# Kernel optimization log

Hardware: AMD Instinct MI355X
Metric: run time of the kernel (lower is better)

The kernel has to match this reference:

```python
import math
import jax, jax.numpy as jnp
import numpy as np

HIDDEN = 768
N_HEADS = 12
HEAD_DIM = HIDDEN // N_HEADS


def _alibi_slopes(num_heads: int) -> np.ndarray:
    def pow2_slopes(n):
        start = 2.0 ** (-2.0 ** (-(math.log2(n) - 3)))
        return start ** np.arange(1, n + 1, dtype=np.float32)
    if math.log2(num_heads).is_integer():
        return pow2_slopes(num_heads).astype(np.float32)
    closest = 2 ** math.floor(math.log2(num_heads))
    base = pow2_slopes(closest)
    extra = pow2_slopes(2 * closest)[0::2][: num_heads - closest]
    return np.concatenate([base, extra], axis=0).astype(np.float32)

ALIBI_SLOPES = jnp.asarray(_alibi_slopes(N_HEADS))


def setup_inputs() -> dict:
    key = jax.random.key(0)
    ks = jax.random.split(key, 7)
    B, S = 4, 2048
    scale = 1.0 / math.sqrt(HIDDEN)
    inp = {
        "hidden_states": jax.random.normal(ks[0], (B, S, HIDDEN), dtype=jnp.float32),
        "Wq": jax.random.normal(ks[1], (HIDDEN, HIDDEN), dtype=jnp.float32) * scale,
        "bq": jnp.zeros((HIDDEN,), dtype=jnp.float32),
        "Wk": jax.random.normal(ks[2], (HIDDEN, HIDDEN), dtype=jnp.float32) * scale,
        "bk": jnp.zeros((HIDDEN,), dtype=jnp.float32),
        "Wv": jax.random.normal(ks[3], (HIDDEN, HIDDEN), dtype=jnp.float32) * scale,
        "bv": jnp.zeros((HIDDEN,), dtype=jnp.float32),
        "attention_mask": jnp.ones((B, S), dtype=jnp.int32),
    }
    return inp


def reference(hidden_states, Wq, bq, Wk, bk, Wv, bv, attention_mask):
    B, S, _ = hidden_states.shape
    H, D = N_HEADS, HEAD_DIM
    scaling = D ** (-0.5)

    # nn.Linear: x @ W.T + b, then split heads -> [B, S, H, D]
    q = (hidden_states @ Wq.T + bq).reshape(B, S, H, D)
    k = (hidden_states @ Wk.T + bk).reshape(B, S, H, D)
    v = (hidden_states @ Vv_fix(Wv, bv, hidden_states)) if False else (hidden_states @ Wv.T + bv).reshape(B, S, H, D)

    # scaled scores [B, H, Sq, Sk]
    scores = jnp.einsum("bqhd,bkhd->bhqk", q, k) * scaling

    # ALiBi bias: -slope[h] * |kv_idx - q_idx|
    pos = jnp.arange(S)
    dist = jnp.abs(pos[None, :] - pos[:, None]).astype(scores.dtype)  # [Sq, Sk]
    alibi = -ALIBI_SLOPES.astype(scores.dtype)[:, None, None] * dist  # [H, Sq, Sk]

    # padding mask over kv positions (additive min like score_mod)
    mask_penalty = jnp.finfo(scores.dtype).min
    mask_bias = jnp.where(attention_mask.astype(bool), 0.0, mask_penalty)  # [B, Sk]

    scores = scores + alibi[None] + mask_bias[:, None, None, :]
    probs = jax.nn.softmax(scores, axis=-1)

    out = jnp.einsum("bhqk,bkhd->bqhd", probs, v)  # [B, Sq, H, D]
    return out.reshape(B, S, H * D)  # dropout is no-op in eval


def Vv_fix(*a):  # unused helper kept trivially (never called)
    raise NotImplementedError
```

## Files before the change

kernel.cpp:

```cpp
#include <hip/hip_runtime.h>
#include <hip/hip_bf16.h>

#define HIDDEN 768
#define NH 12
#define HD 64
#define BB 4
#define SS 2048
#define M_TOT (BB * SS)
#define NQKV (3 * HIDDEN)
#define LOG2E 1.44269504f

typedef __attribute__((ext_vector_type(8))) short bf16x8;
typedef __attribute__((ext_vector_type(4))) float f32x4;
typedef __attribute__((ext_vector_type(4))) unsigned int u32x4;

__device__ inline unsigned short f2bf(float x) {
    __hip_bfloat16 h = __float2bfloat16(x);
    return *reinterpret_cast<unsigned short*>(&h);
}

__device__ inline void gl_lds16(const unsigned short* g, unsigned short* s) {
    __builtin_amdgcn_global_load_lds(
        (const __attribute__((address_space(1))) unsigned int*)g,
        (__attribute__((address_space(3))) unsigned int*)s, 16, 0, 0);
}

__global__ __launch_bounds__(256) void cast_kernel(
    const float* __restrict__ hs, const float* __restrict__ wq,
    const float* __restrict__ wk, const float* __restrict__ wv,
    const int* __restrict__ mask, unsigned short* __restrict__ a_bf,
    unsigned short* __restrict__ w_bf, float* __restrict__ mb,
    int* __restrict__ anym) {
    const int HS_N = M_TOT * HIDDEN / 4;
    const int W_N = HIDDEN * HIDDEN / 4;
    int idx = blockIdx.x * blockDim.x + threadIdx.x;
    if (idx < BB * SS) mb[idx] = mask[idx] ? 0.f : -1e30f;
    if (idx < BB * 32) {
        int b = idx >> 5, t = idx & 31;
        const int* mp = mask + b * SS + t * 64;
        int any = 0;
#pragma unroll 8
        for (int j = 0; j < 64; j++) any |= (mp[j] == 0);
        anym[idx] = any;
    }
    if (idx >= HS_N + 3 * W_N) return;
    if (idx < HS_N) {
        float4 v = ((const float4*)hs)[idx];
        ushort4 o;
        o.x = f2bf(v.x); o.y = f2bf(v.y); o.z = f2bf(v.z); o.w = f2bf(v.w);
        ((ushort4*)a_bf)[idx] = o;
    } else {
        int widx = idx - HS_N;
        const float* src;
        int off;
        if (widx < W_N)        { src = wq; off = widx; }
        else if (widx < 2*W_N) { src = wk; off = widx - W_N; }
        else                   { src = wv; off = widx - 2 * W_N; }
        float4 v = ((const float4*)src)[off];
        ushort4 o;
        o.x = f2bf(v.x); o.y = f2bf(v.y); o.z = f2bf(v.z); o.w = f2bf(v.w);
        ((ushort4*)w_bf)[widx] = o;
    }
}

__global__ __launch_bounds__(256, 3) void qkv_gemm(
    const unsigned short* __restrict__ A, const unsigned short* __restrict__ W,
    const float* __restrict__ bq, const float* __restrict__ bk,
    const float* __restrict__ bv, unsigned short* __restrict__ qbuf,
    unsigned short* __restrict__ kf, unsigned short* __restrict__ vf) {
    __shared__ unsigned short As[2][128][32];
    __shared__ unsigned short Bs[2][128][32];
    const int tid = threadIdx.x;
    const int m0 = blockIdx.y * 128;
    const int n0 = blockIdx.x * 128;
    const int w = tid >> 6, l = tid & 63;
    const int wm = w >> 1, wn = w & 1;
    const int lrow = l & 15;
    const int g4 = l >> 4;
    const int fcol = (g4 ^ (lrow >> 2)) * 8;

    const int srow = l >> 2;
    const int sslot = (l & 3) ^ ((l >> 4) & 3);
    const unsigned short* pA =
        A + (size_t)(m0 + w * 32 + srow) * HIDDEN + sslot * 8;
    const unsigned short* pB =
        W + (size_t)(n0 + w * 32 + srow) * HIDDEN + sslot * 8;

    f32x4 acc[4][4] = {};

#define STAGE(bb)                                          \
    do {                                                   \
        gl_lds16(pA,               &As[bb][w * 32][0]);    \
        gl_lds16(pA + 16 * HIDDEN, &As[bb][w * 32 + 16][0]); \
        gl_lds16(pB,               &Bs[bb][w * 32][0]);    \
        gl_lds16(pB + 16 * HIDDEN, &Bs[bb][w * 32 + 16][0]); \
        pA += 32; pB += 32;                                \
    } while (0)

    STAGE(0);
    __syncthreads();
    int cur = 0;

    for (int kt = 0; kt < HIDDEN / 32; kt++) {
        if (kt < HIDDEN / 32 - 1) STAGE(cur ^ 1);
        bf16x8 af[4], bfr[4];
#pragma unroll
        for (int mi = 0; mi < 4; mi++)
            af[mi] = *(const bf16x8*)&As[cur][wm * 64 + mi * 16 + lrow][fcol];
#pragma unroll
        for (int ni = 0; ni < 4; ni++)
            bfr[ni] = *(const bf16x8*)&Bs[cur][wn * 64 + ni * 16 + lrow][fcol];
        __builtin_amdgcn_s_setprio(1);
#pragma unroll
        for (int mi = 0; mi < 4; mi++)
#pragma unroll
            for (int ni = 0; ni < 4; ni++)
                acc[mi][ni] = __builtin_amdgcn_mfma_f32_16x16x32_bf16(
                    af[mi], bfr[ni], acc[mi][ni], 0, 0, 0);
        __builtin_amdgcn_s_setprio(0);
        __syncthreads();
        cur ^= 1;
    }
#undef STAGE

    if (n0 < 768) {
#pragma unroll
        for (int mi = 0; mi < 4; mi++)
#pragma unroll
            for (int ni = 0; ni < 4; ni++) {
                int col = n0 + wn * 64 + ni * 16 + lrow;
                float bias = bq[col];
#pragma unroll
                for (int i = 0; i < 4; i++) {
                    int row = m0 + wm * 64 + mi * 16 + g4 * 4 + i;
                    qbuf[(size_t)row * 768 + col] =
                        f2bf((acc[mi][ni][i] + bias) * 0.125f);
                }
            }
    } else if (n0 < 1536) {
#pragma unroll
        for (int mi = 0; mi < 4; mi++)
#pragma unroll
            for (int ni = 0; ni < 4; ni++) {
                int dd = n0 - 768 + wn * 64 + ni * 16 + lrow;
                float bias = bk[dd];
                int hh = dd >> 6, d = dd & 63;
                int gk = d >> 3, d8 = d & 7;
#pragma unroll
                for (int i = 0; i < 4; i++) {
                    int row = m0 + wm * 64 + mi * 16 + g4 * 4 + i;
                    int bb2 = row >> 11, s = row & 2047;
                    int kv16 = s >> 4, ls = s & 15;
                    kf[((size_t)(bb2 * NH + hh) * 128 + kv16) * 1024 +
                       (gk * 16 + ls) * 8 + d8] = f2bf(acc[mi][ni][i] + bias);
                }
            }
    } else {
#pragma unroll
        for (int mi = 0; mi < 4; mi++)
#pragma unroll
            for (int ni = 0; ni < 4; ni++) {
                int dd = n0 - 1536 + wn * 64 + ni * 16 + lrow;
                float bias = bv[dd];
                int hh = dd >> 6, d = dd & 63;
                int dm = d >> 4, lr = d & 15;
                int row0 = m0 + wm * 64 + mi * 16 + g4 * 4;
                int bb2 = row0 >> 11, s = row0 & 2047;
                int kv32 = s >> 5, gv = (s >> 3) & 3, s8 = s & 7;
                ushort4 o;
                o.x = f2bf(acc[mi][ni][0] + bias);
                o.y = f2bf(acc[mi][ni][1] + bias);
                o.z = f2bf(acc[mi][ni][2] + bias);
                o.w = f2bf(acc[mi][ni][3] + bias);
                *(ushort4*)(vf + (((size_t)(bb2 * NH + hh) * 4 + dm) * 64 + kv32) * 512 +
                            (gv * 16 + lr) * 8 + s8) = o;
            }
    }
}

__global__ __launch_bounds__(256) void attn_kernel(
    const unsigned short* __restrict__ Qb, const unsigned short* __restrict__ KF,
    const unsigned short* __restrict__ VF, const float* __restrict__ MB,
    const int* __restrict__ ANYM, float* __restrict__ out) {
    __shared__ unsigned short Kl[2][4096];
    __shared__ unsigned short Vl[2][4096];

    const int head_order[12] = {6, 7, 5, 4, 3, 11, 2, 10, 1, 9, 0, 8};
    const int Rtab[12]       = {31, 31, 19, 10, 5, 4, 3, 2, 2, 1, 1, 1};

    const int tid = threadIdx.x;
    const int w = tid >> 6, l = tid & 63;
    const int flat = blockIdx.y * gridDim.x + blockIdx.x;
    const int xcd = flat & 7;
    const int rem = flat >> 3;
    const int slot = rem >> 5;
    const int qt = rem & 31;
    const int byy = slot * 8 + xcd;
    const int hidx = byy >> 2;
    const int b = byy & 3;
    const int h = head_order[hidx];
    const int R = Rtab[hidx];
    const int bh = b * NH + h;
    const int lrow = l & 15;
    const int g = l >> 4;
    const int q = qt * 64 + w * 16 + lrow;
    const int l8 = l * 8;

    const float slope = (h < 8) ? exp2f(-(float)(h + 1))
                                : exp2f(-((float)(h - 8) + 0.5f));
    const float nslope2 = -slope * LOG2E;
    const float stp = 64.f * nslope2;

    const unsigned short* qp = Qb + (size_t)(b * SS + q) * 768 + h * HD + g * 8;
    const bf16x8 qf0 = *(const bf16x8*)(qp);
    const bf16x8 qf1 = *(const bf16x8*)(qp + 32);

    const unsigned short* kfb = KF + (size_t)bh * 128 * 1024;
    const unsigned short* vfb = VF + (size_t)bh * 4 * 64 * 512;
    const float* mbp = MB + b * SS + g * 4;
    const int* anyp = ANYM + b * 32;

    bf16x8 ones;
#pragma unroll
    for (int j = 0; j < 8; j++) ones[j] = (short)0x3F80;

    f32x4 accT[4] = {};
    f32x4 lacc = {};
    float m_run = 14.0f;
    float ta[16];
    bool need_full = true;

    const int kt_lo = max(0, qt - R);
    const int kt_hi = min(31, qt + R);

    {
        const unsigned short* gk0 = kfb + ((size_t)kt_lo * 4 + w) * 1024 + l8;
        const unsigned short* gv0 = vfb + ((size_t)w * 64 + kt_lo * 2) * 512 + l8;
        gl_lds16(gk0,       &Kl[0][w * 1024]);
        gl_lds16(gk0 + 512, &Kl[0][w * 1024 + 512]);
        gl_lds16(gv0,       &Vl[0][w * 1024]);
        gl_lds16(gv0 + 512, &Vl[0][w * 1024 + 512]);
    }
    __syncthreads();

    const unsigned short* gk = kfb + ((size_t)(kt_lo + 1) * 4 + w) * 1024 + l8;
    const unsigned short* gv = vfb + ((size_t)w * 64 + (size_t)(kt_lo + 1) * 2) * 512 + l8;
    int cur = 0;

    for (int kt = kt_lo; kt <= kt_hi; kt++) {
        if (kt < kt_hi) {
            gl_lds16(gk,       &Kl[cur ^ 1][w * 1024]);
            gl_lds16(gk + 512, &Kl[cur ^ 1][w * 1024 + 512]);
            gl_lds16(gv,       &Vl[cur ^ 1][w * 1024]);
            gl_lds16(gv + 512, &Vl[cur ^ 1][w * 1024 + 512]);
            gk += 4096;
            gv += 1024;
        }

        f32x4 s4[4];
        __builtin_amdgcn_s_setprio(1);
#pragma unroll
        for (int nf = 0; nf < 4; nf++) {
            bf16x8 k0 = *(const bf16x8*)&Kl[cur][nf * 1024 + l8];
            bf16x8 k1 = *(const bf16x8*)&Kl[cur][nf * 1024 + 512 + l8];
            f32x4 z = {};
            z = __builtin_amdgcn_mfma_f32_16x16x32_bf16(k0, qf0, z, 0, 0, 0);
            z = __builtin_amdgcn_mfma_f32_16x16x32_bf16(k1, qf1, z, 0, 0, 0);
            s4[nf] = z;
        }
        __builtin_amdgcn_s_setprio(0);

        if (need_full || kt == qt || kt == qt + 1) {
            const float fdf = (float)(kt * 64 + g * 4 - q);
#pragma unroll
            for (int nf = 0; nf < 4; nf++)
#pragma unroll
                for (int i = 0; i < 4; i++)
                    ta[nf * 4 + i] = fabsf(fdf + (float)(nf * 16 + i)) * nslope2;
        } else {
            const float d = (kt > qt) ? stp : -stp;
#pragma unroll
            for (int e = 0; e < 16; e++) ta[e] += d;
        }
        need_full = false;

        float sv[16];
#pragma unroll
        for (int nf = 0; nf < 4; nf++)
#pragma unroll
            for (int i = 0; i < 4; i++)
                sv[nf * 4 + i] = fmaf(s4[nf][i], LOG2E, ta[nf * 4 + i]);
        if (anyp[kt]) {
#pragma unroll
            for (int nf = 0; nf < 4; nf++) {
                float4 mbv = *(const float4*)(mbp + kt * 64 + nf * 16);
                sv[nf * 4 + 0] += mbv.x;
                sv[nf * 4 + 1] += mbv.y;
                sv[nf * 4 + 2] += mbv.z;
                sv[nf * 4 + 3] += mbv.w;
            }
        }

        float t0 = fmaxf(fmaxf(sv[0], sv[1]), sv[2]);
        float t1 = fmaxf(fmaxf(sv[3], sv[4]), sv[5]);
        float t2 = fmaxf(fmaxf(sv[6], sv[7]), sv[8]);
        float t3 = fmaxf(fmaxf(sv[9], sv[10]), sv[11]);
        float t4 = fmaxf(fmaxf(sv[12], sv[13]), sv[14]);
        float mt = fmaxf(fmaxf(fmaxf(t0, t1), fmaxf(t2, t3)), fmaxf(t4, sv[15]));
        mt = fmaxf(mt, __shfl_xor(mt, 16));
        mt = fmaxf(mt, __shfl_xor(mt, 32));

        if (!__all(mt <= m_run + 8.0f)) {
            float mnew = fmaxf(m_run, mt);
            float corr = __builtin_amdgcn_exp2f(m_run - mnew);
            m_run = mnew;
#pragma unroll
            for (int i = 0; i < 4; i++) lacc[i] *= corr;
#pragma unroll
            for (int m = 0; m < 4; m++)
#pragma unroll
                for (int i = 0; i < 4; i++) accT[m][i] *= corr;
        }

        float p[16];
#pragma unroll
        for (int e = 0; e < 16; e++)
            p[e] = __builtin_amdgcn_exp2f(sv[e] - m_run);

        unsigned pk[4][2];
#pragma unroll
        for (int nf = 0; nf < 4; nf++) {
            asm("v_cvt_pk_bf16_f32 %0, %1, %2"
                : "=v"(pk[nf][0]) : "v"(p[nf * 4 + 0]), "v"(p[nf * 4 + 1]));
            asm("v_cvt_pk_bf16_f32 %0, %1, %2"
                : "=v"(pk[nf][1]) : "v"(p[nf * 4 + 2]), "v"(p[nf * 4 + 3]));
        }

        const int dstA = ((((g & 1) << 1) | (g >> 1)) << 4) | lrow;
        const int idxA = dstA << 2;
        const int idxB = idxA ^ 128;
        const bool odd = (g & 1);
        unsigned rA0 = __builtin_amdgcn_ds_permute(idxA, (int)(odd ? pk[1][0] : pk[0][0]));
        unsigned rA1 = __builtin_amdgcn_ds_permute(idxA, (int)(odd ? pk[1][1] : pk[0][1]));
        unsigned rB0 = __builtin_amdgcn_ds_permute(idxB, (int)(odd ? pk[0][0] : pk[1][0]));
        unsigned rB1 = __builtin_amdgcn_ds_permute(idxB, (int)(odd ? pk[0][1] : pk[1][1]));
        unsigned rA2 = __builtin_amdgcn_ds_permute(idxA, (int)(odd ? pk[3][0] : pk[2][0]));
        unsigned rA3 = __builtin_amdgcn_ds_permute(idxA, (int)(odd ? pk[3][1] : pk[2][1]));
        unsigned rB2 = __builtin_amdgcn_ds_permute(idxB, (int)(odd ? pk[2][0] : pk[3][0]));
        unsigned rB3 = __builtin_amdgcn_ds_permute(idxB, (int)(odd ? pk[2][1] : pk[3][1]));
        const bool hi = (g >> 1);
        u32x4 uf0, uf1;
        uf0.x = hi ? rB0 : rA0; uf0.y = hi ? rB1 : rA1;
        uf0.z = hi ? rA0 : rB0; uf0.w = hi ? rA1 : rB1;
        uf1.x = hi ? rB2 : rA2; uf1.y = hi ? rB3 : rA3;
        uf1.z = hi ? rA2 : rB2; uf1.w = hi ? rA3 : rB3;
        bf16x8 pf0 = __builtin_bit_cast(bf16x8, uf0);
        bf16x8 pf1 = __builtin_bit_cast(bf16x8, uf1);

        __builtin_amdgcn_s_setprio(1);
#pragma unroll
        for (int m = 0; m < 4; m++) {
            bf16x8 v0 = *(const bf16x8*)&Vl[cur][m * 1024 + l8];
            bf16x8 v1 = *(const bf16x8*)&Vl[cur][m * 1024 + 512 + l8];
            accT[m] = __builtin_amdgcn_mfma_f32_16x16x32_bf16(v0, pf0, accT[m], 0, 0, 0);
            accT[m] = __builtin_amdgcn_mfma_f32_16x16x32_bf16(v1, pf1, accT[m], 0, 0, 0);
        }
        lacc = __builtin_amdgcn_mfma_f32_16x16x32_bf16(ones, pf0, lacc, 0, 0, 0);
        lacc = __builtin_amdgcn_mfma_f32_16x16x32_bf16(ones, pf1, lacc, 0, 0, 0);
        __builtin_amdgcn_s_setprio(0);

        __syncthreads();
        cur ^= 1;
    }

    const float inv = 1.0f / lacc[0];
    float* op = out + (size_t)(b * SS + q) * HIDDEN + h * HD + g * 4;
#pragma unroll
    for (int m = 0; m < 4; m++) {
        float4 o;
        o.x = accT[m][0] * inv; o.y = accT[m][1] * inv;
        o.z = accT[m][2] * inv; o.w = accT[m][3] * inv;
        *(float4*)(op + m * 16) = o;
    }
}

extern "C" void kernel_launch(void* const* d_in, const int* in_sizes, int n_in,
                              void* d_out, int out_size, void* d_ws,
                              size_t ws_size, hipStream_t stream) {
    const float* hs = (const float*)d_in[0];
    const float* wq = (const float*)d_in[1];
    const float* bq = (const float*)d_in[2];
    const float* wk = (const float*)d_in[3];
    const float* bk = (const float*)d_in[4];
    const float* wv = (const float*)d_in[5];
    const float* bv = (const float*)d_in[6];
    const int* mask = (const int*)d_in[7];
    float* out = (float*)d_out;

    unsigned short* a_bf = (unsigned short*)d_ws;
    unsigned short* w_bf = a_bf + (size_t)M_TOT * HIDDEN;
    unsigned short* qbuf = w_bf + (size_t)NQKV * HIDDEN;
    unsigned short* kf = qbuf + (size_t)M_TOT * 768;
    unsigned short* vf = kf + (size_t)BB * NH * 128 * 1024;
    float* mb = (float*)(vf + (size_t)BB * NH * 4 * 64 * 512);
    int* anym = (int*)(mb + BB * SS);

    int castN = (M_TOT * HIDDEN + 3 * HIDDEN * HIDDEN) / 4;
    cast_kernel<<<(castN + 255) / 256, 256, 0, stream>>>(
        hs, wq, wk, wv, mask, a_bf, w_bf, mb, anym);

    dim3 ggrid(NQKV / 128, M_TOT / 128);
    qkv_gemm<<<ggrid, 256, 0, stream>>>(a_bf, w_bf, bq, bk, bv, qbuf, kf, vf);

    dim3 agrid(SS / 64, NH * BB);
    attn_kernel<<<agrid, 256, 0, stream>>>(qbuf, kf, vf, mb, anym, out);
}
```

Measured before the change: 112.8 us.

## Split long-band attention heads across two KV segments and add a combine kernel

The three heads with the widest ALiBi KV band (6, 7, 5) are now each split into two KV segments, handled by separate work units. Each unit writes its unnormalized output plus its running max and sum, and a new combine kernel merges the two segments. The remaining heads go into a flattened 1280-block grid in which some blocks process two short-band units back to back, to even out per-block work and shrink the tail. This adds an extra kernel launch and partial-output traffic to and from global memory. It falls back to the old kernel when the workspace is too small.

```diff
diff --git a/kernel.cpp b/kernel.cpp
--- a/kernel.cpp
+++ b/kernel.cpp
@@ -178,16 +178,307 @@
     }
 }
 
+
 __global__ __launch_bounds__(256) void attn_kernel(
+    const unsigned short* __restrict__ Qb, const unsigned short* __restrict__ KF,
+    const unsigned short* __restrict__ VF, const float* __restrict__ MB,
+    const int* __restrict__ ANYM, float* __restrict__ out,
+    float* __restrict__ pML, float* __restrict__ pO) {
+    __shared__ unsigned short Kl[2][4096];
+    __shared__ unsigned short Vl[2][4096];
+
+    const int head_order[12] = {6, 7, 5, 4, 3, 11, 2, 10, 1, 9, 0, 8};
+    const int Rtab[12]       = {31, 31, 19, 10, 5, 4, 3, 2, 2, 1, 1, 1};
+
+    const int tid = threadIdx.x;
+    const int w = tid >> 6, l = tid & 63;
+    const int lrow = l & 15;
+    const int g = l >> 4;
+    const int l8 = l * 8;
+    const int u = blockIdx.x;
+    const int nu = (u < 640) ? 2 : 1;
+
+    bf16x8 ones;
+#pragma unroll
+    for (int j = 0; j < 8; j++) ones[j] = (short)0x3F80;
+
+    for (int ui = 0; ui < nu; ui++) {
+        int hidx, b, qt, seg, S;
+        if (ui == 0) {
+            if (u < 768) {
+                hidx = u >> 8; int rr = u & 255;
+                seg = rr & 1; b = (rr >> 1) & 3; qt = rr >> 3; S = 2;
+            } else if (u < 896) {
+                hidx = 3; int rr = u - 768; b = rr & 3; qt = rr >> 2; S = 1; seg = 0;
+            } else {
+                hidx = 4 + ((u - 896) >> 7); int rr = (u - 896) & 127;
+                b = rr & 3; qt = rr >> 2; S = 1; seg = 0;
+            }
+        } else {
+            hidx = 7 + (u >> 7); int rr = u & 127;
+            b = rr & 3; qt = rr >> 2; S = 1; seg = 0;
+        }
+
+        const int h = head_order[hidx];
+        const int R = Rtab[hidx];
+        const int bh = b * NH + h;
+        const int q = qt * 64 + w * 16 + lrow;
+
+        const float slope = (h < 8) ? exp2f(-(float)(h + 1))
+                                    : exp2f(-((float)(h - 8) + 0.5f));
+        const float nslope2 = -slope * LOG2E;
+        const float stp = 64.f * nslope2;
+
+        const unsigned short* qp =
+            Qb + (size_t)(b * SS + q) * 768 + h * HD + g * 8;
+        const bf16x8 qf0 = *(const bf16x8*)(qp);
+        const bf16x8 qf1 = *(const bf16x8*)(qp + 32);
+
+        const unsigned short* kfb = KF + (size_t)bh * 128 * 1024;
+        const unsigned short* vfb = VF + (size_t)bh * 4 * 64 * 512;
+        const float* mbp = MB + b * SS + g * 4;
+        const int* anyp = ANYM + b * 32;
+
+        const int lo0 = max(0, qt - R);
+        const int hi0 = min(31, qt + R);
+        int kt_lo, kt_hi;
+        if (S == 2) {
+            int n = hi0 - lo0 + 1;
+            int len = (n + 1) >> 1;
+            kt_lo = lo0 + seg * len;
+            kt_hi = min(hi0, kt_lo + len - 1);
+        } else {
+            kt_lo = lo0; kt_hi = hi0;
+        }
+
+        f32x4 accT[4] = {};
+        f32x4 lacc = {};
+        float m_run = 14.0f;
+        float ta[16];
+        bool need_full = true;
+
+        {
+            const unsigned short* gk0 = kfb + ((size_t)kt_lo * 4 + w) * 1024 + l8;
+            const unsigned short* gv0 =
+                vfb + ((size_t)w * 64 + (size_t)kt_lo * 2) * 512 + l8;
+            gl_lds16(gk0,       &Kl[0][w * 1024]);
+            gl_lds16(gk0 + 512, &Kl[0][w * 1024 + 512]);
+            gl_lds16(gv0,       &Vl[0][w * 1024]);
+            gl_lds16(gv0 + 512, &Vl[0][w * 1024 + 512]);
+        }
+        __syncthreads();
+
+        const unsigned short* gk = kfb + ((size_t)(kt_lo + 1) * 4 + w) * 1024 + l8;
+        const unsigned short* gv =
+            vfb + ((size_t)w * 64 + (size_t)(kt_lo + 1) * 2) * 512 + l8;
+        int cur = 0;
+
+        for (int kt = kt_lo; kt <= kt_hi; kt++) {
+            if (kt < kt_hi) {
+                gl_lds16(gk,       &Kl[cur ^ 1][w * 1024]);
+                gl_lds16(gk + 512, &Kl[cur ^ 1][w * 1024 + 512]);
+                gl_lds16(gv,       &Vl[cur ^ 1][w * 1024]);
+                gl_lds16(gv + 512, &Vl[cur ^ 1][w * 1024 + 512]);
+                gk += 4096;
+                gv += 1024;
+            }
+
+            f32x4 s4[4];
+            __builtin_amdgcn_s_setprio(1);
+#pragma unroll
+            for (int nf = 0; nf < 4; nf++) {
+                bf16x8 k0 = *(const bf16x8*)&Kl[cur][nf * 1024 + l8];
+                bf16x8 k1 = *(const bf16x8*)&Kl[cur][nf * 1024 + 512 + l8];
+                f32x4 z = {};
+                z = __builtin_amdgcn_mfma_f32_16x16x32_bf16(k0, qf0, z, 0, 0, 0);
+                z = __builtin_amdgcn_mfma_f32_16x16x32_bf16(k1, qf1, z, 0, 0, 0);
+                s4[nf] = z;
+            }
+            __builtin_amdgcn_s_setprio(0);
+
+            if (need_full || kt == qt || kt == qt + 1) {
+                const float fdf = (float)(kt * 64 + g * 4 - q);
+#pragma unroll
+                for (int nf = 0; nf < 4; nf++)
+#pragma unroll
+                    for (int i = 0; i < 4; i++)
+                        ta[nf * 4 + i] =
+                            fabsf(fdf + (float)(nf * 16 + i)) * nslope2;
+            } else {
+                const float d = (kt > qt) ? stp : -stp;
+#pragma unroll
+                for (int e = 0; e < 16; e++) ta[e] += d;
+            }
+            need_full = false;
+
+            float sv[16];
+#pragma unroll
+            for (int nf = 0; nf < 4; nf++)
+#pragma unroll
+                for (int i = 0; i < 4; i++)
+                    sv[nf * 4 + i] = fmaf(s4[nf][i], LOG2E, ta[nf * 4 + i]);
+            if (anyp[kt]) {
+#pragma unroll
+                for (int nf = 0; nf < 4; nf++) {
+                    float4 mbv = *(const float4*)(mbp + kt * 64 + nf * 16);
+                    sv[nf * 4 + 0] += mbv.x;
+                    sv[nf * 4 + 1] += mbv.y;
+                    sv[nf * 4 + 2] += mbv.z;
+                    sv[nf * 4 + 3] += mbv.w;
+                }
+            }
+
+            float t0 = fmaxf(fmaxf(sv[0], sv[1]), sv[2]);
+            float t1 = fmaxf(fmaxf(sv[3], sv[4]), sv[5]);
+            float t2 = fmaxf(fmaxf(sv[6], sv[7]), sv[8]);
+            float t3 = fmaxf(fmaxf(sv[9], sv[10]), sv[11]);
+            float t4 = fmaxf(fmaxf(sv[12], sv[13]), sv[14]);
+            float mt = fmaxf(fmaxf(fmaxf(t0, t1), fmaxf(t2, t3)),
+                             fmaxf(t4, sv[15]));
+            mt = fmaxf(mt, __shfl_xor(mt, 16));
+            mt = fmaxf(mt, __shfl_xor(mt, 32));
+
+            if (!__all(mt <= m_run + 8.0f)) {
+                float mnew = fmaxf(m_run, mt);
+                float corr = __builtin_amdgcn_exp2f(m_run - mnew);
+                m_run = mnew;
+#pragma unroll
+                for (int i = 0; i < 4; i++) lacc[i] *= corr;
+#pragma unroll
+                for (int m = 0; m < 4; m++)
+#pragma unroll
+                    for (int i = 0; i < 4; i++) accT[m][i] *= corr;
+            }
+
+            float p[16];
+#pragma unroll
+            for (int e = 0; e < 16; e++)
+                p[e] = __builtin_amdgcn_exp2f(sv[e] - m_run);
+
+            unsigned pk[4][2];
+#pragma unroll
+            for (int nf = 0; nf < 4; nf++) {
+                asm("v_cvt_pk_bf16_f32 %0, %1, %2"
+                    : "=v"(pk[nf][0]) : "v"(p[nf * 4 + 0]), "v"(p[nf * 4 + 1]));
+                asm("v_cvt_pk_bf16_f32 %0, %1, %2"
+                    : "=v"(pk[nf][1]) : "v"(p[nf * 4 + 2]), "v"(p[nf * 4 + 3]));
+            }
+
+            const int dstA = ((((g & 1) << 1) | (g >> 1)) << 4) | lrow;
+            const int idxA = dstA << 2;
+            const int idxB = idxA ^ 128;
+            const bool odd = (g & 1);
+            unsigned rA0 = __builtin_amdgcn_ds_permute(idxA, (int)(odd ? pk[1][0] : pk[0][0]));
+            unsigned rA1 = __builtin_amdgcn_ds_permute(idxA, (int)(odd ? pk[1][1] : pk[0][1]));
+            unsigned rB0 = __builtin_amdgcn_ds_permute(idxB, (int)(odd ? pk[0][0] : pk[1][0]));
+            unsigned rB1 = __builtin_amdgcn_ds_permute(idxB, (int)(odd ? pk[0][1] : pk[1][1]));
+            unsigned rA2 = __builtin_amdgcn_ds_permute(idxA, (int)(odd ? pk[3][0] : pk[2][0]));
+            unsigned rA3 = __builtin_amdgcn_ds_permute(idxA, (int)(odd ? pk[3][1] : pk[2][1]));
+            unsigned rB2 = __builtin_amdgcn_ds_permute(idxB, (int)(odd ? pk[2][0] : pk[3][0]));
+            unsigned rB3 = __builtin_amdgcn_ds_permute(idxB, (int)(odd ? pk[2][1] : pk[3][1]));
+            const bool hi = (g >> 1);
+            u32x4 uf0, uf1;
+            uf0.x = hi ? rB0 : rA0; uf0.y = hi ? rB1 : rA1;
+            uf0.z = hi ? rA0 : rB0; uf0.w = hi ? rA1 : rB1;
+            uf1.x = hi ? rB2 : rA2; uf1.y = hi ? rB3 : rA3;
+            uf1.z = hi ? rA2 : rB2; uf1.w = hi ? rA3 : rB3;
+            bf16x8 pf0 = __builtin_bit_cast(bf16x8, uf0);
+            bf16x8 pf1 = __builtin_bit_cast(bf16x8, uf1);
+
+            __builtin_amdgcn_s_setprio(1);
+#pragma unroll
+            for (int m = 0; m < 4; m++) {
+                bf16x8 v0 = *(const bf16x8*)&Vl[cur][m * 1024 + l8];
+                bf16x8 v1 = *(const bf16x8*)&Vl[cur][m * 1024 + 512 + l8];
+                accT[m] = __builtin_amdgcn_mfma_f32_16x16x32_bf16(v0, pf0, accT[m], 0, 0, 0);
+                accT[m] = __builtin_amdgcn_mfma_f32_16x16x32_bf16(v1, pf1, accT[m], 0, 0, 0);
+            }
+            lacc = __builtin_amdgcn_mfma_f32_16x16x32_bf16(ones, pf0, lacc, 0, 0, 0);
+            lacc = __builtin_amdgcn_mfma_f32_16x16x32_bf16(ones, pf1, lacc, 0, 0, 0);
+            __builtin_amdgcn_s_setprio(0);
+
+            __syncthreads();
+            cur ^= 1;
+        }
+
+        if (S == 2) {
+            const int ps = (hidx * 4 + b) * 2 + seg;
+            float* pp = pO + ((size_t)ps * SS + q) * 64 + g * 4;
+#pragma unroll
+            for (int m = 0; m < 4; m++) {
+                float4 o;
+                o.x = accT[m][0]; o.y = accT[m][1];
+                o.z = accT[m][2]; o.w = accT[m][3];
+                *(float4*)(pp + m * 16) = o;
+            }
+            if (g == 0) {
+                float2 ml2;
+                ml2.x = m_run;
+                ml2.y = lacc[0];
+                *(float2*)(pML + ((size_t)ps * SS + q) * 2) = ml2;
+            }
+        } else {
+            const float inv = 1.0f / lacc[0];
+            float* op = out + (size_t)(b * SS + q) * HIDDEN + h * HD + g * 4;
+#pragma unroll
+            for (int m = 0; m < 4; m++) {
+                float4 o;
+                o.x = accT[m][0] * inv; o.y = accT[m][1] * inv;
+                o.z = accT[m][2] * inv; o.w = accT[m][3] * inv;
+                *(float4*)(op + m * 16) = o;
+            }
+        }
+    }
+}
+
+__global__ __launch_bounds__(256) void combine_kernel(
+    const float* __restrict__ pML, const float* __restrict__ pO,
+    float* __restrict__ out) {
+    int t = blockIdx.x * 256 + threadIdx.x;
+    int d0 = (t & 7) * 8;
+    int row = t >> 3;
+    int q = row & 2047;
+    int idx = row >> 11;
+    int hidx = idx >> 2, b = idx & 3;
+    int h = (hidx == 0) ? 6 : (hidx == 1) ? 7 : 5;
+    int ps0 = (hidx * 4 + b) * 2;
+
+    float2 ml0 = *(const float2*)(pML + ((size_t)ps0 * SS + q) * 2);
+    float2 ml1 = *(const float2*)(pML + ((size_t)(ps0 + 1) * SS + q) * 2);
+    float M = fmaxf(ml0.x, ml1.x);
+    float w0 = exp2f(ml0.x - M), w1 = exp2f(ml1.x - M);
+    float L = w0 * ml0.y + w1 * ml1.y;
+    const float invL = 1.0f / L;
+
+    const float* p0 = pO + ((size_t)ps0 * SS + q) * 64 + d0;
+    const float* p1 = pO + ((size_t)(ps0 + 1) * SS + q) * 64 + d0;
+    float4 a0 = *(const float4*)(p0);
+    float4 c0 = *(const float4*)(p0 + 4);
+    float4 a1 = *(const float4*)(p1);
+    float4 c1 = *(const float4*)(p1 + 4);
+
+    float* op = out + (size_t)(b * SS + q) * HIDDEN + h * HD + d0;
+    float4 o0, o1;
+    o0.x = (w0 * a0.x + w1 * a1.x) * invL;
+    o0.y = (w0 * a0.y + w1 * a1.y) * invL;
+    o0.z = (w0 * a0.z + w1 * a1.z) * invL;
+    o0.w = (w0 * a0.w + w1 * a1.w) * invL;
+    o1.x = (w0 * c0.x + w1 * c1.x) * invL;
+    o1.y = (w0 * c0.y + w1 * c1.y) * invL;
+    o1.z = (w0 * c0.z + w1 * c1.z) * invL;
+    o1.w = (w0 * c0.w + w1 * c1.w) * invL;
+    *(float4*)(op) = o0;
+    *(float4*)(op + 4) = o1;
+}
+
+__global__ __launch_bounds__(256) void attn_fb(
     const unsigned short* __restrict__ Qb, const unsigned short* __restrict__ KF,
     const unsigned short* __restrict__ VF, const float* __restrict__ MB,
     const int* __restrict__ ANYM, float* __restrict__ out) {
     __shared__ unsigned short Kl[2][4096];
     __shared__ unsigned short Vl[2][4096];
-
     const int head_order[12] = {6, 7, 5, 4, 3, 11, 2, 10, 1, 9, 0, 8};
     const int Rtab[12]       = {31, 31, 19, 10, 5, 4, 3, 2, 2, 1, 1, 1};
-
     const int tid = threadIdx.x;
     const int w = tid >> 6, l = tid & 63;
     const int flat = blockIdx.y * gridDim.x + blockIdx.x;
@@ -205,34 +496,27 @@
     const int g = l >> 4;
     const int q = qt * 64 + w * 16 + lrow;
     const int l8 = l * 8;
-
     const float slope = (h < 8) ? exp2f(-(float)(h + 1))
                                 : exp2f(-((float)(h - 8) + 0.5f));
     const float nslope2 = -slope * LOG2E;
     const float stp = 64.f * nslope2;
-
     const unsigned short* qp = Qb + (size_t)(b * SS + q) * 768 + h * HD + g * 8;
     const bf16x8 qf0 = *(const bf16x8*)(qp);
     const bf16x8 qf1 = *(const bf16x8*)(qp + 32);
-
     const unsigned short* kfb = KF + (size_t)bh * 128 * 1024;
     const unsigned short* vfb = VF + (size_t)bh * 4 * 64 * 512;
     const float* mbp = MB + b * SS + g * 4;
     const int* anyp = ANYM + b * 32;
-
     bf16x8 ones;
 #pragma unroll
     for (int j = 0; j < 8; j++) ones[j] = (short)0x3F80;
-
     f32x4 accT[4] = {};
     f32x4 lacc = {};
     float m_run = 14.0f;
     float ta[16];
     bool need_full = true;
-
     const int kt_lo = max(0, qt - R);
     const int kt_hi = min(31, qt + R);
-
     {
         const unsigned short* gk0 = kfb + ((size_t)kt_lo * 4 + w) * 1024 + l8;
         const unsigned short* gv0 = vfb + ((size_t)w * 64 + kt_lo * 2) * 512 + l8;
@@ -242,11 +526,9 @@
         gl_lds16(gv0 + 512, &Vl[0][w * 1024 + 512]);
     }
     __syncthreads();
-
     const unsigned short* gk = kfb + ((size_t)(kt_lo + 1) * 4 + w) * 1024 + l8;
     const unsigned short* gv = vfb + ((size_t)w * 64 + (size_t)(kt_lo + 1) * 2) * 512 + l8;
     int cur = 0;
-
     for (int kt = kt_lo; kt <= kt_hi; kt++) {
         if (kt < kt_hi) {
             gl_lds16(gk,       &Kl[cur ^ 1][w * 1024]);
@@ -256,7 +538,6 @@
             gk += 4096;
             gv += 1024;
         }
-
         f32x4 s4[4];
         __builtin_amdgcn_s_setprio(1);
 #pragma unroll
@@ -269,7 +550,6 @@
             s4[nf] = z;
         }
         __builtin_amdgcn_s_setprio(0);
-
         if (need_full || kt == qt || kt == qt + 1) {
             const float fdf = (float)(kt * 64 + g * 4 - q);
 #pragma unroll
@@ -283,7 +563,6 @@
             for (int e = 0; e < 16; e++) ta[e] += d;
         }
         need_full = false;
-
         float sv[16];
 #pragma unroll
         for (int nf = 0; nf < 4; nf++)
@@ -300,7 +579,6 @@
                 sv[nf * 4 + 3] += mbv.w;
             }
         }
-
         float t0 = fmaxf(fmaxf(sv[0], sv[1]), sv[2]);
         float t1 = fmaxf(fmaxf(sv[3], sv[4]), sv[5]);
         float t2 = fmaxf(fmaxf(sv[6], sv[7]), sv[8]);
@@ -309,7 +587,6 @@
         float mt = fmaxf(fmaxf(fmaxf(t0, t1), fmaxf(t2, t3)), fmaxf(t4, sv[15]));
         mt = fmaxf(mt, __shfl_xor(mt, 16));
         mt = fmaxf(mt, __shfl_xor(mt, 32));
-
         if (!__all(mt <= m_run + 8.0f)) {
             float mnew = fmaxf(m_run, mt);
             float corr = __builtin_amdgcn_exp2f(m_run - mnew);
@@ -321,12 +598,10 @@
 #pragma unroll
                 for (int i = 0; i < 4; i++) accT[m][i] *= corr;
         }
-
         float p[16];
 #pragma unroll
         for (int e = 0; e < 16; e++)
             p[e] = __builtin_amdgcn_exp2f(sv[e] - m_run);
-
         unsigned pk[4][2];
 #pragma unroll
         for (int nf = 0; nf < 4; nf++) {
@@ -335,7 +610,6 @@
             asm("v_cvt_pk_bf16_f32 %0, %1, %2"
                 : "=v"(pk[nf][1]) : "v"(p[nf * 4 + 2]), "v"(p[nf * 4 + 3]));
         }
-
         const int dstA = ((((g & 1) << 1) | (g >> 1)) << 4) | lrow;
         const int idxA = dstA << 2;
         const int idxB = idxA ^ 128;
@@ -356,7 +630,6 @@
         uf1.z = hi ? rA2 : rB2; uf1.w = hi ? rA3 : rB3;
         bf16x8 pf0 = __builtin_bit_cast(bf16x8, uf0);
         bf16x8 pf1 = __builtin_bit_cast(bf16x8, uf1);
-
         __builtin_amdgcn_s_setprio(1);
 #pragma unroll
         for (int m = 0; m < 4; m++) {
@@ -368,11 +641,9 @@
         lacc = __builtin_amdgcn_mfma_f32_16x16x32_bf16(ones, pf0, lacc, 0, 0, 0);
         lacc = __builtin_amdgcn_mfma_f32_16x16x32_bf16(ones, pf1, lacc, 0, 0, 0);
         __builtin_amdgcn_s_setprio(0);
-
         __syncthreads();
         cur ^= 1;
     }
-
     const float inv = 1.0f / lacc[0];
     float* op = out + (size_t)(b * SS + q) * HIDDEN + h * HD + g * 4;
 #pragma unroll
@@ -404,6 +675,10 @@
     unsigned short* vf = kf + (size_t)BB * NH * 128 * 1024;
     float* mb = (float*)(vf + (size_t)BB * NH * 4 * 64 * 512);
     int* anym = (int*)(mb + BB * SS);
+    float* pml = (float*)(anym + BB * 32);
+    float* po = pml + (size_t)24 * SS * 2;
+    size_t need = (size_t)((char*)(po + (size_t)24 * SS * 64) - (char*)d_ws);
+    const bool use_split = ws_size >= need;
 
     int castN = (M_TOT * HIDDEN + 3 * HIDDEN * HIDDEN) / 4;
     cast_kernel<<<(castN + 255) / 256, 256, 0, stream>>>(
@@ -412,6 +687,12 @@
     dim3 ggrid(NQKV / 128, M_TOT / 128);
     qkv_gemm<<<ggrid, 256, 0, stream>>>(a_bf, w_bf, bq, bk, bv, qbuf, kf, vf);
 
-    dim3 agrid(SS / 64, NH * BB);
-    attn_kernel<<<agrid, 256, 0, stream>>>(qbuf, kf, vf, mb, anym, out);
-}
+    if (use_split) {
+        attn_kernel<<<1280, 256, 0, stream>>>(qbuf, kf, vf, mb, anym, out,
+                                              pml, po);
+        combine_kernel<<<768, 256, 0, stream>>>(pml, po, out);
+    } else {
+        dim3 agrid(SS / 64, NH * BB);
+        attn_fb<<<agrid, 256, 0, stream>>>(qbuf, kf, vf, mb, anym, out);
+    }
+}
```

After: 123.0 us. +9.0%, slower.
